# Optimization experiments

Hardware: AMD Instinct MI355X
Metric: run time of the kernel (lower is better)

The kernel has to match this reference:

```python
import jax, jax.numpy as jnp
import numpy as np

B = 2
C = 256
NH = 8
DH = C // NH
NL = 4
NP = 4
NLAYERS = 6
DFF = 1024
SHAPES = [(128, 128), (64, 64), (32, 32), (16, 16)]
LQ = sum(h * w for h, w in SHAPES)
STARTS = np.cumsum([0] + [h * w for h, w in SHAPES])[:-1].tolist()


def _ln(x, g, b, eps=1e-5):
    mu = jnp.mean(x, -1, keepdims=True)
    var = jnp.mean((x - mu) ** 2, -1, keepdims=True)
    return (x - mu) * jax.lax.rsqrt(var + eps) * g + b


def _ref_points():
    # centers of each cell, normalized to [0,1]; valid_ratios == 1 (masks=None path)
    pts = []
    for (h, w) in SHAPES:
        ry = (np.arange(h) + 0.5) / h
        rx = (np.arange(w) + 0.5) / w
        gy, gx = np.meshgrid(ry, rx, indexing='ij')
        pts.append(np.stack([gx.reshape(-1), gy.reshape(-1)], -1))
    return jnp.asarray(np.concatenate(pts, 0), jnp.float32)  # [LQ,2] (x,y)


def _bilinear(vf, loc, Hl, Wl):
    # vf: [B,NH,S,DH] flattened level features; loc: [B,LQ,NH,NP,2] in [0,1]
    # grid_sample semantics: bilinear, zero padding, align_corners=False
    x = loc[..., 0] * Wl - 0.5
    y = loc[..., 1] * Hl - 0.5
    x0 = jnp.floor(x)
    y0 = jnp.floor(y)
    wx = x - x0
    wy = y - y0
    out = 0.0
    for dx, dy, w in ((0, 0, (1 - wx) * (1 - wy)), (1, 0, wx * (1 - wy)),
                      (0, 1, (1 - wx) * wy), (1, 1, wx * wy)):
        xi = x0 + dx
        yi = y0 + dy
        valid = (xi >= 0) & (xi < Wl) & (yi >= 0) & (yi < Hl)
        idx = (jnp.clip(yi, 0, Hl - 1) * Wl + jnp.clip(xi, 0, Wl - 1)).astype(jnp.int32)
        idx = jnp.transpose(idx, (0, 2, 1, 3)).reshape(B, NH, -1)  # [B,NH,LQ*NP]
        g = jnp.take_along_axis(vf, idx[..., None], axis=2)        # [B,NH,LQ*NP,DH]
        wgt = jnp.transpose(w * valid, (0, 2, 1, 3)).reshape(B, NH, -1)
        out = out + g * wgt[..., None]
    return out.reshape(B, NH, LQ, NP, DH)


def _forward(src0, src1, src2, src3, pos0, pos1, pos2, pos3, level_embed,
             Woff, boff, Wattn, battn, Wval, bval, Wout, bout,
             g1, b1, Wff1, bff1, Wff2, bff2, g2, b2):
    srcs = [src0, src1, src2, src3]
    poss = [pos0, pos1, pos2, pos3]
    src = jnp.concatenate([s.reshape(B, C, -1).transpose(0, 2, 1) for s in srcs], 1)
    pos = jnp.concatenate([p.reshape(B, C, -1).transpose(0, 2, 1) + level_embed[l][None, None]
                           for l, p in enumerate(poss)], 1)
    ref = _ref_points()  # [LQ,2]
    norm_wh = jnp.asarray([[w, h] for (h, w) in SHAPES], jnp.float32)  # offset_normalizer
    x = src
    for l in range(NLAYERS):
        q = x + pos
        off = (q @ Woff[l] + boff[l]).reshape(B, LQ, NH, NL, NP, 2)
        attn = jax.nn.softmax((q @ Wattn[l] + battn[l]).reshape(B, LQ, NH, NL * NP), -1)
        attn = attn.reshape(B, LQ, NH, NL, NP)
        val = (x @ Wval[l] + bval[l]).reshape(B, LQ, NH, DH)
        loc = ref[None, :, None, None, None, :] + off / norm_wh[None, None, None, :, None, :]
        out = jnp.zeros((B, NH, LQ, DH), x.dtype)
        for lv, (h, w) in enumerate(SHAPES):
            s0 = STARTS[lv]
            vf = val[:, s0:s0 + h * w].transpose(0, 2, 1, 3)   # [B,NH,S,DH]
            samp = _bilinear(vf, loc[:, :, :, lv], h, w)       # [B,NH,LQ,NP,DH]
            a = attn[:, :, :, lv].transpose(0, 2, 1, 3)        # [B,NH,LQ,NP]
            out = out + jnp.einsum('bhqpd,bhqp->bhqd', samp, a)
        out = out.transpose(0, 2, 1, 3).reshape(B, LQ, C) @ Wout[l] + bout[l]
        x = _ln(x + out, g1[l], b1[l])
        ff = jax.nn.relu(x @ Wff1[l] + bff1[l]) @ Wff2[l] + bff2[l]
        x = _ln(x + ff, g2[l], b2[l])
    return x


def setup_inputs() -> dict:
    key = jax.random.key(0)
    ks = jax.random.split(key, 20)
    d = {}
    for i, (h, w) in enumerate(SHAPES):
        d[f'src{i}'] = jax.random.normal(ks[i], (B, C, h, w), jnp.float32)
        d[f'pos{i}'] = jax.random.normal(ks[4 + i], (B, C, h, w), jnp.float32) * 0.1
    d['level_embed'] = jax.random.normal(ks[8], (NL, C), jnp.float32)

    def lin(k, fi, fo, scale=None):
        s = scale if scale is not None else 1.0 / np.sqrt(fi)
        return jax.random.normal(k, (NLAYERS, fi, fo), jnp.float32) * s

    d['Woff'] = lin(ks[9], C, NH * NL * NP * 2, 0.01)
    d['boff'] = jax.random.uniform(ks[10], (NLAYERS, NH * NL * NP * 2), jnp.float32, -0.5, 0.5)
    d['Wattn'] = lin(ks[11], C, NH * NL * NP)
    d['battn'] = jnp.zeros((NLAYERS, NH * NL * NP), jnp.float32)
    d['Wval'] = lin(ks[12], C, C)
    d['bval'] = jnp.zeros((NLAYERS, C), jnp.float32)
    d['Wout'] = lin(ks[13], C, C)
    d['bout'] = jnp.zeros((NLAYERS, C), jnp.float32)
    d['g1'] = jnp.ones((NLAYERS, C), jnp.float32)
    d['b1'] = jnp.zeros((NLAYERS, C), jnp.float32)
    d['Wff1'] = lin(ks[14], C, DFF)
    d['bff1'] = jnp.zeros((NLAYERS, DFF), jnp.float32)
    d['Wff2'] = lin(ks[15], DFF, C)
    d['bff2'] = jnp.zeros((NLAYERS, C), jnp.float32)
    d['g2'] = jnp.ones((NLAYERS, C), jnp.float32)
    d['b2'] = jnp.zeros((NLAYERS, C), jnp.float32)
    return d


def reference(src0, src1, src2, src3, pos0, pos1, pos2, pos3, level_embed,
              Woff, boff, Wattn, battn, Wval, bval, Wout, bout,
              g1, b1, Wff1, bff1, Wff2, bff2, g2, b2):
    return _forward(src0, src1, src2, src3, pos0, pos1, pos2, pos3, level_embed,
                    Woff, boff, Wattn, battn, Wval, bval, Wout, bout,
                    g1, b1, Wff1, bff1, Wff2, bff2, g2, b2)
```

## Files before the change

### kernel.cpp

```cpp
#include <hip/hip_runtime.h>
#include <hip/hip_bf16.h>
#include <hip/hip_fp16.h>
#include <math.h>

namespace {
constexpr int B_   = 2;
constexpr int C_   = 256;
constexpr int NH_  = 8;
constexpr int DH_  = 32;
constexpr int NP_  = 4;
constexpr int DFF_ = 1024;
constexpr int LQ_  = 21760;
constexpr int M_   = B_ * LQ_;
}

typedef __bf16  bf16x8 __attribute__((ext_vector_type(8)));
typedef short   s16x8  __attribute__((ext_vector_type(8)));
typedef float   f32x4  __attribute__((ext_vector_type(4)));

#define AS1 __attribute__((address_space(1)))
#define AS3 __attribute__((address_space(3)))

static __device__ __forceinline__ unsigned short f2bf(float f) {
    return __builtin_bit_cast(unsigned short, __float2bfloat16(f));
}
static __device__ __forceinline__ float bf2f(unsigned short u) {
    return __bfloat162float(__builtin_bit_cast(__hip_bfloat16, u));
}

__global__ void k_wt(const float* __restrict__ in, __hip_bfloat16* __restrict__ out,
                     int K, int N, int outStride)
{
    __shared__ float tile[32][33];
    int n0 = blockIdx.x * 32, k0 = blockIdx.y * 32;
    const float* inl = in + (size_t)blockIdx.z * K * N;
    __hip_bfloat16* outl = out + (size_t)blockIdx.z * outStride;
    for (int i = threadIdx.y; i < 32; i += 8)
        tile[i][threadIdx.x] = inl[(size_t)(k0 + i) * N + n0 + threadIdx.x];
    __syncthreads();
    for (int i = threadIdx.y; i < 32; i += 8)
        outl[(size_t)(n0 + i) * K + k0 + threadIdx.x] = __float2bfloat16(tile[threadIdx.x][i]);
}

__global__ __launch_bounds__(256) void k_assemble2(
    const float* __restrict__ s0, const float* __restrict__ s1,
    const float* __restrict__ s2, const float* __restrict__ s3,
    const float* __restrict__ p0, const float* __restrict__ p1,
    const float* __restrict__ p2, const float* __restrict__ p3,
    const float* __restrict__ lev, float* __restrict__ x,
    __hip_bfloat16* __restrict__ xbf, __hip_bfloat16* __restrict__ posbf,
    __hip_bfloat16* __restrict__ qbf)
{
    int bid = blockIdx.x;
    int lv, rem, HW, S0;
    const float *sp, *pp;
    if (bid < 8192)       { lv = 0; rem = bid;         HW = 16384; S0 = 0;     sp = s0; pp = p0; }
    else if (bid < 10240) { lv = 1; rem = bid - 8192;  HW = 4096;  S0 = 16384; sp = s1; pp = p1; }
    else if (bid < 10752) { lv = 2; rem = bid - 10240; HW = 1024;  S0 = 20480; sp = s2; pp = p2; }
    else                  { lv = 3; rem = bid - 10752; HW = 256;   S0 = 21504; sp = s3; pp = p3; }
    int sptiles = HW >> 5;
    int spt = rem % sptiles;
    int ct  = (rem / sptiles) & 7;
    int b   = rem / (sptiles * 8);
    int sp0 = spt * 32, c0 = ct * 32;

    __shared__ float ts[32][33], tp[32][33];
    int tx = threadIdx.x & 31, ty = threadIdx.x >> 5;
#pragma unroll
    for (int i = 0; i < 4; i++) {
        int c = c0 + ty + i * 8;
        size_t si = ((size_t)(b * C_ + c)) * HW + sp0 + tx;
        ts[ty + i * 8][tx] = sp[si];
        tp[ty + i * 8][tx] = pp[si];
    }
    __syncthreads();
#pragma unroll
    for (int i = 0; i < 4; i++) {
        int s = S0 + sp0 + ty + i * 8;
        int c = c0 + tx;
        float sv = ts[tx][ty + i * 8];
        float pv = tp[tx][ty + i * 8] + lev[lv * C_ + c];
        size_t idx = ((size_t)(b * LQ_ + s)) * C_ + c;
        x[idx]     = sv;
        xbf[idx]   = __float2bfloat16(sv);
        posbf[idx] = __float2bfloat16(pv);
        qbf[idx]   = __float2bfloat16(sv + pv);
    }
}

template<bool RELU, bool BF16OUT>
__global__ __launch_bounds__(256) void k_gemm_mfma(
    const __hip_bfloat16* __restrict__ A,
    const __hip_bfloat16* __restrict__ Wt,
    const float* __restrict__ bias,
    void* __restrict__ Co,
    int M, int N, int K)
{
    __shared__ char As[128 * 128];
    __shared__ char Bs[128 * 128];
    int t = threadIdx.x, w = t >> 6, lane = t & 63;
    int m0 = blockIdx.x * 128, n0 = blockIdx.y * 128;
    int wm = w >> 1, wn = w & 1;

    f32x4 acc[4][4] = {};

    int rowoff  = lane >> 3;
    int colswz  = ((lane & 7) ^ (lane >> 3)) << 3;

    for (int kt = 0; kt < K; kt += 64) {
#pragma unroll
        for (int j = 0; j < 4; j++) {
            int rowbase = w * 32 + j * 8;
            const __hip_bfloat16* srcA = A  + (size_t)(m0 + rowbase + rowoff) * K + kt + colswz;
            const __hip_bfloat16* srcB = Wt + (size_t)(n0 + rowbase + rowoff) * K + kt + colswz;
            __builtin_amdgcn_global_load_lds(
                (const AS1 void*)srcA, (AS3 void*)(As + rowbase * 128), 16, 0, 0);
            __builtin_amdgcn_global_load_lds(
                (const AS1 void*)srcB, (AS3 void*)(Bs + rowbase * 128), 16, 0, 0);
        }
        __syncthreads();
#pragma unroll
        for (int k0 = 0; k0 < 64; k0 += 32) {
            int kb = k0 * 2 + (lane >> 4) * 16;
            bf16x8 af[4], bfr[4];
#pragma unroll
            for (int mi = 0; mi < 4; mi++) {
                int r = wm * 64 + mi * 16 + (lane & 15);
                s16x8 raw = *(const s16x8*)(As + r * 128 + (kb ^ ((r & 7) << 4)));
                af[mi] = __builtin_bit_cast(bf16x8, raw);
            }
#pragma unroll
            for (int ni = 0; ni < 4; ni++) {
                int r = wn * 64 + ni * 16 + (lane & 15);
                s16x8 raw = *(const s16x8*)(Bs + r * 128 + (kb ^ ((r & 7) << 4)));
                bfr[ni] = __builtin_bit_cast(bf16x8, raw);
            }
#pragma unroll
            for (int mi = 0; mi < 4; mi++)
#pragma unroll
                for (int ni = 0; ni < 4; ni++)
                    acc[mi][ni] = __builtin_amdgcn_mfma_f32_16x16x32_bf16(
                        af[mi], bfr[ni], acc[mi][ni], 0, 0, 0);
        }
        __syncthreads();
    }

#pragma unroll
    for (int ni = 0; ni < 4; ni++) {
        int col = n0 + wn * 64 + ni * 16 + (lane & 15);
        float bb = bias[col];
#pragma unroll
        for (int mi = 0; mi < 4; mi++) {
            int row = m0 + wm * 64 + mi * 16 + ((lane >> 4) << 2);
#pragma unroll
            for (int r = 0; r < 4; r++) {
                float v = acc[mi][ni][r] + bb;
                if (RELU) v = fmaxf(v, 0.f);
                if (BF16OUT)
                    ((__hip_bfloat16*)Co)[(size_t)(row + r) * N + col] = __float2bfloat16(v);
                else
                    ((float*)Co)[(size_t)(row + r) * N + col] = v;
            }
        }
    }
}

__global__ __launch_bounds__(256) void k_gemm_qa(
    const __hip_bfloat16* __restrict__ A,
    const __hip_bfloat16* __restrict__ Wq,
    const float* __restrict__ boff, const float* __restrict__ battn,
    __half* __restrict__ offh, float* __restrict__ attb, int M)
{
    constexpr int K = 256;
    __shared__ char As[128 * 128];
    __shared__ char Bs[128 * 128];
    int t = threadIdx.x, w = t >> 6, lane = t & 63;
    int m0 = blockIdx.x * 128, n0 = blockIdx.y * 128;
    int wm = w >> 1, wn = w & 1;

    f32x4 acc[4][4] = {};
    int rowoff  = lane >> 3;
    int colswz  = ((lane & 7) ^ (lane >> 3)) << 3;

    for (int kt = 0; kt < K; kt += 64) {
#pragma unroll
        for (int j = 0; j < 4; j++) {
            int rowbase = w * 32 + j * 8;
            const __hip_bfloat16* srcA = A  + (size_t)(m0 + rowbase + rowoff) * K + kt + colswz;
            const __hip_bfloat16* srcB = Wq + (size_t)(n0 + rowbase + rowoff) * K + kt + colswz;
            __builtin_amdgcn_global_load_lds(
                (const AS1 void*)srcA, (AS3 void*)(As + rowbase * 128), 16, 0, 0);
            __builtin_amdgcn_global_load_lds(
                (const AS1 void*)srcB, (AS3 void*)(Bs + rowbase * 128), 16, 0, 0);
        }
        __syncthreads();
#pragma unroll
        for (int k0 = 0; k0 < 64; k0 += 32) {
            int kb = k0 * 2 + (lane >> 4) * 16;
            bf16x8 af[4], bfr[4];
#pragma unroll
            for (int mi = 0; mi < 4; mi++) {
                int r = wm * 64 + mi * 16 + (lane & 15);
                s16x8 raw = *(const s16x8*)(As + r * 128 + (kb ^ ((r & 7) << 4)));
                af[mi] = __builtin_bit_cast(bf16x8, raw);
            }
#pragma unroll
            for (int ni = 0; ni < 4; ni++) {
                int r = wn * 64 + ni * 16 + (lane & 15);
                s16x8 raw = *(const s16x8*)(Bs + r * 128 + (kb ^ ((r & 7) << 4)));
                bfr[ni] = __builtin_bit_cast(bf16x8, raw);
            }
#pragma unroll
            for (int mi = 0; mi < 4; mi++)
#pragma unroll
                for (int ni = 0; ni < 4; ni++)
                    acc[mi][ni] = __builtin_amdgcn_mfma_f32_16x16x32_bf16(
                        af[mi], bfr[ni], acc[mi][ni], 0, 0, 0);
        }
        __syncthreads();
    }

    if (blockIdx.y == 2) {
#pragma unroll
        for (int ni = 0; ni < 4; ni++) {
            int col = wn * 64 + ni * 16 + (lane & 15);
            float bb = battn[col];
#pragma unroll
            for (int mi = 0; mi < 4; mi++) {
                int row = m0 + wm * 64 + mi * 16 + ((lane >> 4) << 2);
#pragma unroll
                for (int r = 0; r < 4; r++)
                    attb[(size_t)(row + r) * 128 + col] = acc[mi][ni][r] + bb;
            }
        }
    } else {
#pragma unroll
        for (int ni = 0; ni < 4; ni++) {
            int col = n0 + wn * 64 + ni * 16 + (lane & 15);
            float bb = boff[col];
#pragma unroll
            for (int mi = 0; mi < 4; mi++) {
                int row = m0 + wm * 64 + mi * 16 + ((lane >> 4) << 2);
#pragma unroll
                for (int r = 0; r < 4; r++)
                    offh[(size_t)(row + r) * 256 + col] = __float2half(acc[mi][ni][r] + bb);
            }
        }
    }
}

template<bool WRITE_Q>
static __device__ __forceinline__ void ln_epilogue64(
    f32x4 (&acc)[4][4], int m0, int w, int lane,
    const float* bias, float* xio, __hip_bfloat16* xbf,
    const float* g, const float* beta,
    const __hip_bfloat16* posb, __hip_bfloat16* qout,
    float (*sred1)[4], float (*sred2)[4])
{
    int cl = lane & 15;
    int rg = (lane >> 4) << 2;
    float bcol[4], gcol[4], btcol[4];
#pragma unroll
    for (int ni = 0; ni < 4; ni++) {
        int col = w * 64 + ni * 16 + cl;
        bcol[ni]  = bias[col];
        gcol[ni]  = g[col];
        btcol[ni] = beta[col];
    }

#pragma unroll
    for (int mi = 0; mi < 4; mi++)
#pragma unroll
    for (int r = 0; r < 4; r++) {
        int lr  = mi * 16 + rg + r;
        int row = m0 + lr;
        float s = 0.f;
#pragma unroll
        for (int ni = 0; ni < 4; ni++) {
            int col = w * 64 + ni * 16 + cl;
            float v = acc[mi][ni][r] + bcol[ni] + xio[(size_t)row * 256 + col];
            acc[mi][ni][r] = v;
            s += v;
        }
        s += __shfl_xor(s, 1); s += __shfl_xor(s, 2);
        s += __shfl_xor(s, 4); s += __shfl_xor(s, 8);
        if (cl == 0) sred1[lr][w] = s;
    }
    __syncthreads();

    float mu[4][4];
#pragma unroll
    for (int mi = 0; mi < 4; mi++)
#pragma unroll
    for (int r = 0; r < 4; r++) {
        int lr = mi * 16 + rg + r;
        mu[mi][r] = (sred1[lr][0] + sred1[lr][1] + sred1[lr][2] + sred1[lr][3]) * (1.f / 256.f);
        float s2 = 0.f;
#pragma unroll
        for (int ni = 0; ni < 4; ni++) {
            float d = acc[mi][ni][r] - mu[mi][r];
            s2 += d * d;
        }
        s2 += __shfl_xor(s2, 1); s2 += __shfl_xor(s2, 2);
        s2 += __shfl_xor(s2, 4); s2 += __shfl_xor(s2, 8);
        if (cl == 0) sred2[lr][w] = s2;
    }
    __syncthreads();

#pragma unroll
    for (int mi = 0; mi < 4; mi++)
#pragma unroll
    for (int r = 0; r < 4; r++) {
        int lr  = mi * 16 + rg + r;
        int row = m0 + lr;
        float var = (sred2[lr][0] + sred2[lr][1] + sred2[lr][2] + sred2[lr][3]) * (1.f / 256.f);
        float rstd = rsqrtf(var + 1e-5f);
#pragma unroll
        for (int ni = 0; ni < 4; ni++) {
            int col = w * 64 + ni * 16 + cl;
            size_t idx = (size_t)row * 256 + col;
            float o = (acc[mi][ni][r] - mu[mi][r]) * rstd * gcol[ni] + btcol[ni];
            xio[idx] = o;
            xbf[idx] = __float2bfloat16(o);
            if (WRITE_Q)
                qout[idx] = __float2bfloat16(o + bf2f(__builtin_bit_cast(unsigned short, posb[idx])));
        }
    }
}

static __device__ __forceinline__ void stage_x64(
    const __hip_bfloat16* __restrict__ src, int m0, char* xs, int w, int lane)
{
    int r  = lane >> 5;
    int gl = lane & 31;
#pragma unroll
    for (int j = 0; j < 8; j++) {
        int row = (j * 4 + w) * 2 + r;
        int gsw = gl ^ (row & 7);
        const __hip_bfloat16* s = src + (size_t)(m0 + row) * 256 + gsw * 8;
        __builtin_amdgcn_global_load_lds(
            (const AS1 void*)s, (AS3 void*)(xs + (j * 4 + w) * 1024), 16, 0, 0);
    }
}

template<bool WRITE_Q>
__global__ __launch_bounds__(256) void k_out(
    const __hip_bfloat16* __restrict__ A,
    const __hip_bfloat16* __restrict__ Wt,
    const float* __restrict__ bias,
    float* __restrict__ xio, __hip_bfloat16* __restrict__ xbf,
    const float* __restrict__ g, const float* __restrict__ beta,
    const __hip_bfloat16* __restrict__ posb, __hip_bfloat16* __restrict__ qout)
{
    __shared__ char xs[64 * 512];
    __shared__ float sred1[64][4];
    __shared__ float sred2[64][4];

    int t = threadIdx.x, w = t >> 6, lane = t & 63;
    int m0 = blockIdx.x * 64;

    stage_x64(A, m0, xs, w, lane);
    asm volatile("s_waitcnt vmcnt(0)" ::: "memory");
    __builtin_amdgcn_s_barrier();

    f32x4 acc[4][4] = {};
#pragma unroll
    for (int k0 = 0; k0 < 256; k0 += 32) {
        int kb = k0 * 2 + (lane >> 4) * 16;
        bf16x8 af[4], bw[4];
#pragma unroll
        for (int mi = 0; mi < 4; mi++) {
            int r = mi * 16 + (lane & 15);
            s16x8 raw = *(const s16x8*)(xs + r * 512 + (kb ^ ((r & 7) << 4)));
            af[mi] = __builtin_bit_cast(bf16x8, raw);
        }
#pragma unroll
        for (int ni = 0; ni < 4; ni++) {
            int out = w * 64 + ni * 16 + (lane & 15);
            bw[ni] = *(const bf16x8*)(Wt + (size_t)out * 256 + k0 + (lane >> 4) * 8);
        }
#pragma unroll
        for (int mi = 0; mi < 4; mi++)
#pragma unroll
            for (int ni = 0; ni < 4; ni++)
                acc[mi][ni] = __builtin_amdgcn_mfma_f32_16x16x32_bf16(
                    af[mi], bw[ni], acc[mi][ni], 0, 0, 0);
    }
    __syncthreads();

    ln_epilogue64<WRITE_Q>(acc, m0, w, lane, bias, xio, xbf, g, beta, posb, qout,
                           sred1, sred2);
}

template<bool WRITE_Q>
__global__ __launch_bounds__(256, 2) void k_ff(
    const __hip_bfloat16* __restrict__ xin,
    const __hip_bfloat16* __restrict__ w1t,
    const float* __restrict__ b1v,
    const __hip_bfloat16* __restrict__ w2t,
    const float* __restrict__ b2v,
    float* __restrict__ xio, __hip_bfloat16* __restrict__ xbf,
    const float* __restrict__ g, const float* __restrict__ beta,
    const __hip_bfloat16* __restrict__ posb, __hip_bfloat16* __restrict__ qout)
{
    __shared__ char xs[64 * 512];
    __shared__ char hs[64 * 256];
    __shared__ float sred1[64][4];
    __shared__ float sred2[64][4];

    int t = threadIdx.x, w = t >> 6, lane = t & 63;
    int m0 = blockIdx.x * 64;

    stage_x64(xin, m0, xs, w, lane);
    asm volatile("s_waitcnt vmcnt(0)" ::: "memory");
    __builtin_amdgcn_s_barrier();

    f32x4 acc2[4][4] = {};

    for (int hc = 0; hc < 8; hc++) {
        f32x4 acc1[4][2] = {};
#pragma unroll
        for (int k0 = 0; k0 < 256; k0 += 32) {
            int kb = k0 * 2 + (lane >> 4) * 16;
            bf16x8 af[4], b1f[2];
#pragma unroll
            for (int mi = 0; mi < 4; mi++) {
                int r = mi * 16 + (lane & 15);
                s16x8 raw = *(const s16x8*)(xs + r * 512 + (kb ^ ((r & 7) << 4)));
                af[mi] = __builtin_bit_cast(bf16x8, raw);
            }
#pragma unroll
            for (int ni = 0; ni < 2; ni++) {
                int hid = hc * 128 + w * 32 + ni * 16 + (lane & 15);
                b1f[ni] = *(const bf16x8*)(w1t + (size_t)hid * 256 + k0 + (lane >> 4) * 8);
            }
#pragma unroll
            for (int mi = 0; mi < 4; mi++)
#pragma unroll
                for (int ni = 0; ni < 2; ni++)
                    acc1[mi][ni] = __builtin_amdgcn_mfma_f32_16x16x32_bf16(
                        af[mi], b1f[ni], acc1[mi][ni], 0, 0, 0);
        }

#pragma unroll
        for (int ni = 0; ni < 2; ni++) {
            int hidl = w * 32 + ni * 16 + (lane & 15);
            float bb = b1v[hc * 128 + hidl];
#pragma unroll
            for (int mi = 0; mi < 4; mi++)
#pragma unroll
            for (int r = 0; r < 4; r++) {
                int row = mi * 16 + ((lane >> 4) << 2) + r;
                float v = fmaxf(acc1[mi][ni][r] + bb, 0.f);
                int byte = row * 256 + ((hidl * 2) ^ ((row & 7) << 4));
                *(unsigned short*)(hs + byte) = f2bf(v);
            }
        }
        __syncthreads();

#pragma unroll
        for (int k0 = 0; k0 < 128; k0 += 32) {
            int kb = k0 * 2 + (lane >> 4) * 16;
            bf16x8 ah[4], bw[4];
#pragma unroll
            for (int mi = 0; mi < 4; mi++) {
                int r = mi * 16 + (lane & 15);
                s16x8 raw = *(const s16x8*)(hs + r * 256 + (kb ^ ((r & 7) << 4)));
                ah[mi] = __builtin_bit_cast(bf16x8, raw);
            }
#pragma unroll
            for (int ni = 0; ni < 4; ni++) {
                int out = w * 64 + ni * 16 + (lane & 15);
                bw[ni] = *(const bf16x8*)(w2t + (size_t)out * 1024 + hc * 128 + k0 + (lane >> 4) * 8);
            }
#pragma unroll
            for (int mi = 0; mi < 4; mi++)
#pragma unroll
                for (int ni = 0; ni < 4; ni++)
                    acc2[mi][ni] = __builtin_amdgcn_mfma_f32_16x16x32_bf16(
                        ah[mi], bw[ni], acc2[mi][ni], 0, 0, 0);
        }
        __syncthreads();
    }

    ln_epilogue64<WRITE_Q>(acc2, m0, w, lane, b2v, xio, xbf, g, beta, posb, qout,
                           sred1, sred2);
}

__global__ __launch_bounds__(256) void k_sample4(const __hip_bfloat16* __restrict__ val,
                                                 const __half* __restrict__ offh,
                                                 const float* __restrict__ logits,
                                                 __hip_bfloat16* __restrict__ out)
{
    __shared__ int2 sIW[4 * 64 * 17];

    int t  = threadIdx.x;
    int qb = blockIdx.x;

#pragma unroll
    for (int it = 0; it < 4; it++) {
        int item = t + it * 256;
        int qi = item >> 7;
        int pt = item & 127;
        int bs = qb * 8 + qi;
        int b  = bs / LQ_;
        int s  = bs % LQ_;
        int h  = pt >> 4, lv = (pt >> 2) & 3;

        float lg = logits[(size_t)bs * 128 + pt];
        float mx = lg;
#pragma unroll
        for (int m = 1; m < 16; m <<= 1) mx = fmaxf(mx, __shfl_xor(mx, m));
        float ex = __expf(lg - mx);
        float sm = ex;
#pragma unroll
        for (int m = 1; m < 16; m <<= 1) sm += __shfl_xor(sm, m);
        float aw = ex / sm;

        int p0, Wq;
        if (s < 16384)      { p0 = s;         Wq = 128; }
        else if (s < 20480) { p0 = s - 16384; Wq = 64;  }
        else if (s < 21504) { p0 = s - 20480; Wq = 32;  }
        else                { p0 = s - 21504; Wq = 16;  }
        float invWq = 1.f / (float)Wq;
        float refx = ((p0 % Wq) + 0.5f) * invWq;
        float refy = ((p0 / Wq) + 0.5f) * invWq;

        int W  = 128 >> lv;
        int S0 = (65536 - (65536 >> (2 * lv))) / 3;
        float fW = (float)W;

        __half2 o2 = ((const __half2*)(offh + (size_t)bs * 256))[pt];
        float ox = __low2float(o2), oy = __high2float(o2);
        float xx = refx * fW + ox - 0.5f;
        float yy = refy * fW + oy - 0.5f;
        float x0f = floorf(xx), y0f = floorf(yy);
        float wx = xx - x0f, wy = yy - y0f;
        int x0 = (int)x0f, y0 = (int)y0f;
        int x1 = x0 + 1, y1 = y0 + 1;
        bool vx0 = (x0 >= 0) & (x0 < W), vx1 = (x1 >= 0) & (x1 < W);
        bool vy0 = (y0 >= 0) & (y0 < W), vy1 = (y1 >= 0) & (y1 < W);
        int cx0 = min(max(x0, 0), W - 1), cx1 = min(max(x1, 0), W - 1);
        int cy0 = min(max(y0, 0), W - 1), cy1 = min(max(y1, 0), W - 1);

        int rowbase = (b * LQ_ + S0) * C_ + h * DH_;
        int g  = item >> 4;
        int pj = pt & 15;
        int i00 = (rowbase + (cy0 * W + cx0) * C_) * 2;
        int i10 = (rowbase + (cy0 * W + cx1) * C_) * 2;
        int i01 = (rowbase + (cy1 * W + cx0) * C_) * 2;
        int i11 = (rowbase + (cy1 * W + cx1) * C_) * 2;
        float w00 = aw * (1.f - wx) * (1.f - wy) * ((vx0 & vy0) ? 1.f : 0.f);
        float w10 = aw * wx * (1.f - wy) * ((vx1 & vy0) ? 1.f : 0.f);
        float w01 = aw * (1.f - wx) * wy * ((vx0 & vy1) ? 1.f : 0.f);
        float w11 = aw * wx * wy * ((vx1 & vy1) ? 1.f : 0.f);
        sIW[(0 * 64 + g) * 17 + pj] = make_int2(i00, __float_as_int(w00));
        sIW[(1 * 64 + g) * 17 + pj] = make_int2(i10, __float_as_int(w10));
        sIW[(2 * 64 + g) * 17 + pj] = make_int2(i01, __float_as_int(w01));
        sIW[(3 * 64 + g) * 17 + pj] = make_int2(i11, __float_as_int(w11));
    }
    __syncthreads();

    {
        int g  = t >> 2;
        int dq = t & 3;
        int bs = qb * 8 + (g >> 3);
        int h  = g & 7;
        int dbyte = dq * 16;

        const char* vbase = (const char*)val;
        float a0 = 0.f, a1 = 0.f, a2 = 0.f, a3 = 0.f;
        float a4 = 0.f, a5 = 0.f, a6 = 0.f, a7 = 0.f;
#pragma unroll
        for (int j = 0; j < 16; j++) {
#pragma unroll
            for (int k = 0; k < 4; k++) {
                int2 iw = sIW[(k * 64 + g) * 17 + j];
                float w = __int_as_float(iw.y);
                uint4 u = *(const uint4*)(vbase + iw.x + dbyte);
                a0 = fmaf(w, __builtin_bit_cast(float, u.x << 16), a0);
                a1 = fmaf(w, __builtin_bit_cast(float, u.x & 0xffff0000u), a1);
                a2 = fmaf(w, __builtin_bit_cast(float, u.y << 16), a2);
                a3 = fmaf(w, __builtin_bit_cast(float, u.y & 0xffff0000u), a3);
                a4 = fmaf(w, __builtin_bit_cast(float, u.z << 16), a4);
                a5 = fmaf(w, __builtin_bit_cast(float, u.z & 0xffff0000u), a5);
                a6 = fmaf(w, __builtin_bit_cast(float, u.w << 16), a6);
                a7 = fmaf(w, __builtin_bit_cast(float, u.w & 0xffff0000u), a7);
            }
        }
        uint4 o;
        o.x = (unsigned)f2bf(a0) | ((unsigned)f2bf(a1) << 16);
        o.y = (unsigned)f2bf(a2) | ((unsigned)f2bf(a3) << 16);
        o.z = (unsigned)f2bf(a4) | ((unsigned)f2bf(a5) << 16);
        o.w = (unsigned)f2bf(a6) | ((unsigned)f2bf(a7) << 16);
        *(uint4*)((char*)out + (size_t)bs * 512 + h * 64 + dbyte) = o;
    }
}

extern "C" void kernel_launch(void* const* d_in, const int* in_sizes, int n_in,
                              void* d_out, int out_size, void* d_ws, size_t ws_size,
                              hipStream_t stream)
{
    const float* src_[4] = {(const float*)d_in[0], (const float*)d_in[2],
                            (const float*)d_in[4], (const float*)d_in[6]};
    const float* pos_[4] = {(const float*)d_in[1], (const float*)d_in[3],
                            (const float*)d_in[5], (const float*)d_in[7]};
    const float* lev   = (const float*)d_in[8];
    const float* Woff  = (const float*)d_in[9];
    const float* boff  = (const float*)d_in[10];
    const float* Wattn = (const float*)d_in[11];
    const float* battn = (const float*)d_in[12];
    const float* Wval  = (const float*)d_in[13];
    const float* bval  = (const float*)d_in[14];
    const float* Wout  = (const float*)d_in[15];
    const float* bout  = (const float*)d_in[16];
    const float* g1    = (const float*)d_in[17];
    const float* b1    = (const float*)d_in[18];
    const float* Wff1  = (const float*)d_in[19];
    const float* bff1  = (const float*)d_in[20];
    const float* Wff2  = (const float*)d_in[21];
    const float* bff2  = (const float*)d_in[22];
    const float* g2    = (const float*)d_in[23];
    const float* b2    = (const float*)d_in[24];

    float* x = (float*)d_out;
    size_t MC = (size_t)M_ * C_;

    __hip_bfloat16* pos_bf = (__hip_bfloat16*)d_ws;
    __hip_bfloat16* q_bf   = pos_bf + MC;
    __hip_bfloat16* x_bf   = q_bf + MC;
    __half* offh           = (__half*)(x_bf + MC);
    float*  attb           = (float*)(offh + MC);
    __hip_bfloat16* val_bf = (__hip_bfloat16*)(attb + (size_t)M_ * 128);
    __hip_bfloat16* wbf    = val_bf + MC;

    __hip_bfloat16* wq    = wbf;
    __hip_bfloat16* wvalt = wq    + 6 * 98304;
    __hip_bfloat16* woutt = wvalt + 6 * 65536;
    __hip_bfloat16* wff1t = woutt + 6 * 65536;
    __hip_bfloat16* wff2t = wff1t + 6 * 262144;

    dim3 blk(256);
    dim3 tblk(32, 8);

    k_wt<<<dim3(8, 8, 6),  tblk, 0, stream>>>(Woff,  wq,               256, 256,  98304);
    k_wt<<<dim3(4, 8, 6),  tblk, 0, stream>>>(Wattn, wq + 256 * 256,   256, 128,  98304);
    k_wt<<<dim3(8, 8, 6),  tblk, 0, stream>>>(Wval,  wvalt,            256, 256,  65536);
    k_wt<<<dim3(8, 8, 6),  tblk, 0, stream>>>(Wout,  woutt,            256, 256,  65536);
    k_wt<<<dim3(32, 8, 6), tblk, 0, stream>>>(Wff1,  wff1t,            256, 1024, 262144);
    k_wt<<<dim3(8, 32, 6), tblk, 0, stream>>>(Wff2,  wff2t,            1024, 256, 262144);

    k_assemble2<<<10880, blk, 0, stream>>>(
        src_[0], src_[1], src_[2], src_[3],
        pos_[0], pos_[1], pos_[2], pos_[3], lev, x, x_bf, pos_bf, q_bf);

    for (int l = 0; l < 6; l++) {
        k_gemm_qa<<<dim3(M_ / 128, 3), blk, 0, stream>>>(
            q_bf, wq + (size_t)l * 98304, boff + l * 256, battn + l * 128,
            offh, attb, M_);

        k_gemm_mfma<false, true><<<dim3(M_ / 128, 2), blk, 0, stream>>>(
            x_bf, wvalt + (size_t)l * 65536, bval + l * 256, val_bf, M_, 256, C_);

        k_sample4<<<M_ / 8, blk, 0, stream>>>(val_bf, offh, attb, q_bf);

        k_out<false><<<M_ / 64, blk, 0, stream>>>(
            q_bf, woutt + (size_t)l * 65536, bout + l * 256,
            x, x_bf, g1 + l * 256, b1 + l * 256, nullptr, nullptr);

        if (l < 5)
            k_ff<true><<<M_ / 64, blk, 0, stream>>>(
                x_bf, wff1t + (size_t)l * 262144, bff1 + l * DFF_,
                wff2t + (size_t)l * 262144, bff2 + l * C_,
                x, x_bf, g2 + l * 256, b2 + l * 256, pos_bf, q_bf);
        else
            k_ff<false><<<M_ / 64, blk, 0, stream>>>(
                x_bf, wff1t + (size_t)l * 262144, bff1 + l * DFF_,
                wff2t + (size_t)l * 262144, bff2 + l * C_,
                x, x_bf, g2 + l * 256, b2 + l * 256, nullptr, nullptr);
    }
}
```

Measured before the change: 1.874 ms.

## Split fused FFN into FF1 GEMM plus double-buffered FF2+LayerNorm kernel

Replaces the fully fused FFN kernel, which recomputed the hidden activations chunk by chunk in shared memory, with two kernels. A direct-weight GEMM writes the ReLU hidden activations to global memory in bf16, reusing the offset buffer. A 512-thread, 128-row FF2 kernel with double-buffered LDS staging of A then runs the residual-add and LayerNorm epilogue. The value projection also moves to the same direct-weight 64-row GEMM instead of the LDS-tiled one. This trades an extra global round trip of the hidden tensor for better occupancy and pipelining, and it relies on the offset buffer being free at that point in the layer.

```diff
diff --git a/kernel.cpp b/kernel.cpp
--- a/kernel.cpp
+++ b/kernel.cpp
@@ -88,83 +88,6 @@
     }
 }
 
-template<bool RELU, bool BF16OUT>
-__global__ __launch_bounds__(256) void k_gemm_mfma(
-    const __hip_bfloat16* __restrict__ A,
-    const __hip_bfloat16* __restrict__ Wt,
-    const float* __restrict__ bias,
-    void* __restrict__ Co,
-    int M, int N, int K)
-{
-    __shared__ char As[128 * 128];
-    __shared__ char Bs[128 * 128];
-    int t = threadIdx.x, w = t >> 6, lane = t & 63;
-    int m0 = blockIdx.x * 128, n0 = blockIdx.y * 128;
-    int wm = w >> 1, wn = w & 1;
-
-    f32x4 acc[4][4] = {};
-
-    int rowoff  = lane >> 3;
-    int colswz  = ((lane & 7) ^ (lane >> 3)) << 3;
-
-    for (int kt = 0; kt < K; kt += 64) {
-#pragma unroll
-        for (int j = 0; j < 4; j++) {
-            int rowbase = w * 32 + j * 8;
-            const __hip_bfloat16* srcA = A  + (size_t)(m0 + rowbase + rowoff) * K + kt + colswz;
-            const __hip_bfloat16* srcB = Wt + (size_t)(n0 + rowbase + rowoff) * K + kt + colswz;
-            __builtin_amdgcn_global_load_lds(
-                (const AS1 void*)srcA, (AS3 void*)(As + rowbase * 128), 16, 0, 0);
-            __builtin_amdgcn_global_load_lds(
-                (const AS1 void*)srcB, (AS3 void*)(Bs + rowbase * 128), 16, 0, 0);
-        }
-        __syncthreads();
-#pragma unroll
-        for (int k0 = 0; k0 < 64; k0 += 32) {
-            int kb = k0 * 2 + (lane >> 4) * 16;
-            bf16x8 af[4], bfr[4];
-#pragma unroll
-            for (int mi = 0; mi < 4; mi++) {
-                int r = wm * 64 + mi * 16 + (lane & 15);
-                s16x8 raw = *(const s16x8*)(As + r * 128 + (kb ^ ((r & 7) << 4)));
-                af[mi] = __builtin_bit_cast(bf16x8, raw);
-            }
-#pragma unroll
-            for (int ni = 0; ni < 4; ni++) {
-                int r = wn * 64 + ni * 16 + (lane & 15);
-                s16x8 raw = *(const s16x8*)(Bs + r * 128 + (kb ^ ((r & 7) << 4)));
-                bfr[ni] = __builtin_bit_cast(bf16x8, raw);
-            }
-#pragma unroll
-            for (int mi = 0; mi < 4; mi++)
-#pragma unroll
-                for (int ni = 0; ni < 4; ni++)
-                    acc[mi][ni] = __builtin_amdgcn_mfma_f32_16x16x32_bf16(
-                        af[mi], bfr[ni], acc[mi][ni], 0, 0, 0);
-        }
-        __syncthreads();
-    }
-
-#pragma unroll
-    for (int ni = 0; ni < 4; ni++) {
-        int col = n0 + wn * 64 + ni * 16 + (lane & 15);
-        float bb = bias[col];
-#pragma unroll
-        for (int mi = 0; mi < 4; mi++) {
-            int row = m0 + wm * 64 + mi * 16 + ((lane >> 4) << 2);
-#pragma unroll
-            for (int r = 0; r < 4; r++) {
-                float v = acc[mi][ni][r] + bb;
-                if (RELU) v = fmaxf(v, 0.f);
-                if (BF16OUT)
-                    ((__hip_bfloat16*)Co)[(size_t)(row + r) * N + col] = __float2bfloat16(v);
-                else
-                    ((float*)Co)[(size_t)(row + r) * N + col] = v;
-            }
-        }
-    }
-}
-
 __global__ __launch_bounds__(256) void k_gemm_qa(
     const __hip_bfloat16* __restrict__ A,
     const __hip_bfloat16* __restrict__ Wq,
@@ -249,6 +172,21 @@
     }
 }
 
+static __device__ __forceinline__ void stage_x64(
+    const __hip_bfloat16* __restrict__ src, int m0, char* xs, int w, int lane)
+{
+    int r  = lane >> 5;
+    int gl = lane & 31;
+#pragma unroll
+    for (int j = 0; j < 8; j++) {
+        int row = (j * 4 + w) * 2 + r;
+        int gsw = gl ^ (row & 7);
+        const __hip_bfloat16* s = src + (size_t)(m0 + row) * 256 + gsw * 8;
+        __builtin_amdgcn_global_load_lds(
+            (const AS1 void*)s, (AS3 void*)(xs + (j * 4 + w) * 1024), 16, 0, 0);
+    }
+}
+
 template<bool WRITE_Q>
 static __device__ __forceinline__ void ln_epilogue64(
     f32x4 (&acc)[4][4], int m0, int w, int lane,
@@ -328,18 +266,59 @@
     }
 }
 
-static __device__ __forceinline__ void stage_x64(
-    const __hip_bfloat16* __restrict__ src, int m0, char* xs, int w, int lane)
-{
-    int r  = lane >> 5;
-    int gl = lane & 31;
-#pragma unroll
-    for (int j = 0; j < 8; j++) {
-        int row = (j * 4 + w) * 2 + r;
-        int gsw = gl ^ (row & 7);
-        const __hip_bfloat16* s = src + (size_t)(m0 + row) * 256 + gsw * 8;
-        __builtin_amdgcn_global_load_lds(
-            (const AS1 void*)s, (AS3 void*)(xs + (j * 4 + w) * 1024), 16, 0, 0);
+template<bool RELU>
+__global__ __launch_bounds__(256) void k_gemm_direct(
+    const __hip_bfloat16* __restrict__ A,
+    const __hip_bfloat16* __restrict__ Wt,
+    const float* __restrict__ bias,
+    __hip_bfloat16* __restrict__ out, int N)
+{
+    __shared__ char xs[64 * 512];
+    int t = threadIdx.x, w = t >> 6, lane = t & 63;
+    int m0 = blockIdx.x * 64, n0 = blockIdx.y * 256;
+
+    stage_x64(A, m0, xs, w, lane);
+    asm volatile("s_waitcnt vmcnt(0)" ::: "memory");
+    __builtin_amdgcn_s_barrier();
+
+    f32x4 acc[4][4] = {};
+#pragma unroll
+    for (int k0 = 0; k0 < 256; k0 += 32) {
+        int kb = k0 * 2 + (lane >> 4) * 16;
+        bf16x8 af[4], bw[4];
+#pragma unroll
+        for (int mi = 0; mi < 4; mi++) {
+            int r = mi * 16 + (lane & 15);
+            s16x8 raw = *(const s16x8*)(xs + r * 512 + (kb ^ ((r & 7) << 4)));
+            af[mi] = __builtin_bit_cast(bf16x8, raw);
+        }
+#pragma unroll
+        for (int ni = 0; ni < 4; ni++) {
+            int col = n0 + w * 64 + ni * 16 + (lane & 15);
+            bw[ni] = *(const bf16x8*)(Wt + (size_t)col * 256 + k0 + (lane >> 4) * 8);
+        }
+#pragma unroll
+        for (int mi = 0; mi < 4; mi++)
+#pragma unroll
+            for (int ni = 0; ni < 4; ni++)
+                acc[mi][ni] = __builtin_amdgcn_mfma_f32_16x16x32_bf16(
+                    af[mi], bw[ni], acc[mi][ni], 0, 0, 0);
+    }
+
+#pragma unroll
+    for (int ni = 0; ni < 4; ni++) {
+        int col = n0 + w * 64 + ni * 16 + (lane & 15);
+        float bb = bias[col];
+#pragma unroll
+        for (int mi = 0; mi < 4; mi++) {
+            int row = m0 + mi * 16 + ((lane >> 4) << 2);
+#pragma unroll
+            for (int r = 0; r < 4; r++) {
+                float v = acc[mi][ni][r] + bb;
+                if (RELU) v = fmaxf(v, 0.f);
+                out[(size_t)(row + r) * N + col] = __float2bfloat16(v);
+            }
+        }
     }
 }
 
@@ -376,8 +355,8 @@
         }
 #pragma unroll
         for (int ni = 0; ni < 4; ni++) {
-            int out = w * 64 + ni * 16 + (lane & 15);
-            bw[ni] = *(const bf16x8*)(Wt + (size_t)out * 256 + k0 + (lane >> 4) * 8);
+            int col = w * 64 + ni * 16 + (lane & 15);
+            bw[ni] = *(const bf16x8*)(Wt + (size_t)col * 256 + k0 + (lane >> 4) * 8);
         }
 #pragma unroll
         for (int mi = 0; mi < 4; mi++)
@@ -393,98 +372,144 @@
 }
 
 template<bool WRITE_Q>
-__global__ __launch_bounds__(256, 2) void k_ff(
-    const __hip_bfloat16* __restrict__ xin,
-    const __hip_bfloat16* __restrict__ w1t,
-    const float* __restrict__ b1v,
-    const __hip_bfloat16* __restrict__ w2t,
-    const float* __restrict__ b2v,
+__global__ __launch_bounds__(512) void k_ff2ln(
+    const __hip_bfloat16* __restrict__ A,
+    const __hip_bfloat16* __restrict__ Wt,
+    const float* __restrict__ bias,
     float* __restrict__ xio, __hip_bfloat16* __restrict__ xbf,
     const float* __restrict__ g, const float* __restrict__ beta,
-    const __hip_bfloat16* __restrict__ posb, __hip_bfloat16* __restrict__ qout)
-{
-    __shared__ char xs[64 * 512];
-    __shared__ char hs[64 * 256];
-    __shared__ float sred1[64][4];
-    __shared__ float sred2[64][4];
+    const __hip_bfloat16* __restrict__ posb, __hip_bfloat16* __restrict__ qout,
+    int M, int K)
+{
+    __shared__ char As[2][128 * 128];
+    __shared__ float sred1[128][4];
+    __shared__ float sred2[128][4];
 
     int t = threadIdx.x, w = t >> 6, lane = t & 63;
-    int m0 = blockIdx.x * 64;
-
-    stage_x64(xin, m0, xs, w, lane);
+    int m0 = blockIdx.x * 128;
+    int wm = w >> 2, wn = w & 3;
+
+    f32x4 acc[4][4] = {};
+
+    int rowoff  = lane >> 3;
+    int colswz  = ((lane & 7) ^ rowoff) << 3;
+
+    auto STAGE_A = [&](char* Ab, int kt) {
+#pragma unroll
+        for (int j = 0; j < 2; j++) {
+            int rowbase = w * 16 + j * 8;
+            const __hip_bfloat16* srcA = A + (size_t)(m0 + rowbase + rowoff) * K + kt + colswz;
+            __builtin_amdgcn_global_load_lds(
+                (const AS1 void*)srcA, (AS3 void*)(Ab + rowbase * 128), 16, 0, 0);
+        }
+    };
+
+    STAGE_A(As[0], 0);
     asm volatile("s_waitcnt vmcnt(0)" ::: "memory");
     __builtin_amdgcn_s_barrier();
 
-    f32x4 acc2[4][4] = {};
-
-    for (int hc = 0; hc < 8; hc++) {
-        f32x4 acc1[4][2] = {};
-#pragma unroll
-        for (int k0 = 0; k0 < 256; k0 += 32) {
+    const int nt = K >> 6;
+    int cur = 0;
+    for (int tt = 0; tt < nt; ++tt) {
+        if (tt + 1 < nt) STAGE_A(As[cur ^ 1], (tt + 1) << 6);
+        const char* Ab = As[cur];
+        int ktb = tt << 6;
+#pragma unroll
+        for (int k0 = 0; k0 < 64; k0 += 32) {
             int kb = k0 * 2 + (lane >> 4) * 16;
-            bf16x8 af[4], b1f[2];
+            bf16x8 af[4], bw[4];
 #pragma unroll
             for (int mi = 0; mi < 4; mi++) {
-                int r = mi * 16 + (lane & 15);
-                s16x8 raw = *(const s16x8*)(xs + r * 512 + (kb ^ ((r & 7) << 4)));
+                int r = wm * 64 + mi * 16 + (lane & 15);
+                s16x8 raw = *(const s16x8*)(Ab + r * 128 + (kb ^ ((r & 7) << 4)));
                 af[mi] = __builtin_bit_cast(bf16x8, raw);
             }
 #pragma unroll
-            for (int ni = 0; ni < 2; ni++) {
-                int hid = hc * 128 + w * 32 + ni * 16 + (lane & 15);
-                b1f[ni] = *(const bf16x8*)(w1t + (size_t)hid * 256 + k0 + (lane >> 4) * 8);
+            for (int ni = 0; ni < 4; ni++) {
+                int col = wn * 64 + ni * 16 + (lane & 15);
+                bw[ni] = *(const bf16x8*)(Wt + (size_t)col * K + ktb + k0 + (lane >> 4) * 8);
             }
 #pragma unroll
             for (int mi = 0; mi < 4; mi++)
 #pragma unroll
-                for (int ni = 0; ni < 2; ni++)
-                    acc1[mi][ni] = __builtin_amdgcn_mfma_f32_16x16x32_bf16(
-                        af[mi], b1f[ni], acc1[mi][ni], 0, 0, 0);
-        }
-
-#pragma unroll
-        for (int ni = 0; ni < 2; ni++) {
-            int hidl = w * 32 + ni * 16 + (lane & 15);
-            float bb = b1v[hc * 128 + hidl];
-#pragma unroll
-            for (int mi = 0; mi < 4; mi++)
-#pragma unroll
-            for (int r = 0; r < 4; r++) {
-                int row = mi * 16 + ((lane >> 4) << 2) + r;
-                float v = fmaxf(acc1[mi][ni][r] + bb, 0.f);
-                int byte = row * 256 + ((hidl * 2) ^ ((row & 7) << 4));
-                *(unsigned short*)(hs + byte) = f2bf(v);
-            }
-        }
-        __syncthreads();
-
-#pragma unroll
-        for (int k0 = 0; k0 < 128; k0 += 32) {
-            int kb = k0 * 2 + (lane >> 4) * 16;
-            bf16x8 ah[4], bw[4];
-#pragma unroll
-            for (int mi = 0; mi < 4; mi++) {
-                int r = mi * 16 + (lane & 15);
-                s16x8 raw = *(const s16x8*)(hs + r * 256 + (kb ^ ((r & 7) << 4)));
-                ah[mi] = __builtin_bit_cast(bf16x8, raw);
-            }
-#pragma unroll
-            for (int ni = 0; ni < 4; ni++) {
-                int out = w * 64 + ni * 16 + (lane & 15);
-                bw[ni] = *(const bf16x8*)(w2t + (size_t)out * 1024 + hc * 128 + k0 + (lane >> 4) * 8);
-            }
-#pragma unroll
-            for (int mi = 0; mi < 4; mi++)
-#pragma unroll
                 for (int ni = 0; ni < 4; ni++)
-                    acc2[mi][ni] = __builtin_amdgcn_mfma_f32_16x16x32_bf16(
-                        ah[mi], bw[ni], acc2[mi][ni], 0, 0, 0);
-        }
-        __syncthreads();
-    }
-
-    ln_epilogue64<WRITE_Q>(acc2, m0, w, lane, b2v, xio, xbf, g, beta, posb, qout,
-                           sred1, sred2);
+                    acc[mi][ni] = __builtin_amdgcn_mfma_f32_16x16x32_bf16(
+                        af[mi], bw[ni], acc[mi][ni], 0, 0, 0);
+        }
+        asm volatile("s_waitcnt vmcnt(0)" ::: "memory");
+        __builtin_amdgcn_s_barrier();
+        cur ^= 1;
+    }
+
+    int cl = lane & 15;
+    int rg = (lane >> 4) << 2;
+    float bcol[4], gcol[4], btcol[4];
+#pragma unroll
+    for (int ni = 0; ni < 4; ni++) {
+        int col = wn * 64 + ni * 16 + cl;
+        bcol[ni]  = bias[col];
+        gcol[ni]  = g[col];
+        btcol[ni] = beta[col];
+    }
+
+#pragma unroll
+    for (int mi = 0; mi < 4; mi++)
+#pragma unroll
+    for (int r = 0; r < 4; r++) {
+        int lr  = wm * 64 + mi * 16 + rg + r;
+        int row = m0 + lr;
+        float s = 0.f;
+#pragma unroll
+        for (int ni = 0; ni < 4; ni++) {
+            int col = wn * 64 + ni * 16 + cl;
+            float v = acc[mi][ni][r] + bcol[ni] + xio[(size_t)row * 256 + col];
+            acc[mi][ni][r] = v;
+            s += v;
+        }
+        s += __shfl_xor(s, 1); s += __shfl_xor(s, 2);
+        s += __shfl_xor(s, 4); s += __shfl_xor(s, 8);
+        if (cl == 0) sred1[lr][wn] = s;
+    }
+    __syncthreads();
+
+    float mu[4][4];
+#pragma unroll
+    for (int mi = 0; mi < 4; mi++)
+#pragma unroll
+    for (int r = 0; r < 4; r++) {
+        int lr = wm * 64 + mi * 16 + rg + r;
+        mu[mi][r] = (sred1[lr][0] + sred1[lr][1] + sred1[lr][2] + sred1[lr][3]) * (1.f / 256.f);
+        float s2 = 0.f;
+#pragma unroll
+        for (int ni = 0; ni < 4; ni++) {
+            float d = acc[mi][ni][r] - mu[mi][r];
+            s2 += d * d;
+        }
+        s2 += __shfl_xor(s2, 1); s2 += __shfl_xor(s2, 2);
+        s2 += __shfl_xor(s2, 4); s2 += __shfl_xor(s2, 8);
+        if (cl == 0) sred2[lr][wn] = s2;
+    }
+    __syncthreads();
+
+#pragma unroll
+    for (int mi = 0; mi < 4; mi++)
+#pragma unroll
+    for (int r = 0; r < 4; r++) {
+        int lr  = wm * 64 + mi * 16 + rg + r;
+        int row = m0 + lr;
+        float var = (sred2[lr][0] + sred2[lr][1] + sred2[lr][2] + sred2[lr][3]) * (1.f / 256.f);
+        float rstd = rsqrtf(var + 1e-5f);
+#pragma unroll
+        for (int ni = 0; ni < 4; ni++) {
+            int col = wn * 64 + ni * 16 + cl;
+            size_t idx = (size_t)row * 256 + col;
+            float o = (acc[mi][ni][r] - mu[mi][r]) * rstd * gcol[ni] + btcol[ni];
+            xio[idx] = o;
+            xbf[idx] = __float2bfloat16(o);
+            if (WRITE_Q)
+                qout[idx] = __float2bfloat16(o + bf2f(__builtin_bit_cast(unsigned short, posb[idx])));
+        }
+    }
 }
 
 __global__ __launch_bounds__(256) void k_sample4(const __hip_bfloat16* __restrict__ val,
@@ -632,7 +657,9 @@
     __half* offh           = (__half*)(x_bf + MC);
     float*  attb           = (float*)(offh + MC);
     __hip_bfloat16* val_bf = (__hip_bfloat16*)(attb + (size_t)M_ * 128);
-    __hip_bfloat16* wbf    = val_bf + MC;
+    __hip_bfloat16* pad_bf = val_bf + MC;
+    __hip_bfloat16* ffh_bf = (__hip_bfloat16*)offh;
+    __hip_bfloat16* wbf    = pad_bf + MC;
 
     __hip_bfloat16* wq    = wbf;
     __hip_bfloat16* wvalt = wq    + 6 * 98304;
@@ -659,8 +686,8 @@
             q_bf, wq + (size_t)l * 98304, boff + l * 256, battn + l * 128,
             offh, attb, M_);
 
-        k_gemm_mfma<false, true><<<dim3(M_ / 128, 2), blk, 0, stream>>>(
-            x_bf, wvalt + (size_t)l * 65536, bval + l * 256, val_bf, M_, 256, C_);
+        k_gemm_direct<false><<<dim3(M_ / 64, 1), blk, 0, stream>>>(
+            x_bf, wvalt + (size_t)l * 65536, bval + l * 256, val_bf, 256);
 
         k_sample4<<<M_ / 8, blk, 0, stream>>>(val_bf, offh, attb, q_bf);
 
@@ -668,15 +695,16 @@
             q_bf, woutt + (size_t)l * 65536, bout + l * 256,
             x, x_bf, g1 + l * 256, b1 + l * 256, nullptr, nullptr);
 
+        k_gemm_direct<true><<<dim3(M_ / 64, 4), blk, 0, stream>>>(
+            x_bf, wff1t + (size_t)l * 262144, bff1 + l * DFF_, ffh_bf, DFF_);
+
         if (l < 5)
-            k_ff<true><<<M_ / 64, blk, 0, stream>>>(
-                x_bf, wff1t + (size_t)l * 262144, bff1 + l * DFF_,
-                wff2t + (size_t)l * 262144, bff2 + l * C_,
-                x, x_bf, g2 + l * 256, b2 + l * 256, pos_bf, q_bf);
+            k_ff2ln<true><<<M_ / 128, 512, 0, stream>>>(
+                ffh_bf, wff2t + (size_t)l * 262144, bff2 + l * C_,
+                x, x_bf, g2 + l * 256, b2 + l * 256, pos_bf, q_bf, M_, DFF_);
         else
-            k_ff<false><<<M_ / 64, blk, 0, stream>>>(
-                x_bf, wff1t + (size_t)l * 262144, bff1 + l * DFF_,
-                wff2t + (size_t)l * 262144, bff2 + l * C_,
-                x, x_bf, g2 + l * 256, b2 + l * 256, nullptr, nullptr);
-    }
-}
+            k_ff2ln<false><<<M_ / 128, 512, 0, stream>>>(
+                ffh_bf, wff2t + (size_t)l * 262144, bff2 + l * C_,
+                x, x_bf, g2 + l * 256, b2 + l * 256, nullptr, nullptr, M_, DFF_);
+    }
+}
```

After: 2.188 ms. 16.8% more time.
